# Optimization experiments

Measured on AMD Instinct MI355X. Metric: run time of the kernel, lower is better.

## Reference

```python
import jax, jax.numpy as jnp
import numpy as np

MAX_LENGTH = 128
SOS_TOKEN = 0

V, H, B, S = 16384, 512, 32, 128


def gru_cell(x, h, Wih, Whh, bih, bhh):
    # torch nn.GRU gate layout: [r, z, n]
    gi = x @ Wih.T + bih  # [B, 3H]
    gh = h @ Whh.T + bhh  # [B, 3H]
    ir, iz, inn = jnp.split(gi, 3, axis=-1)
    hr, hz, hn = jnp.split(gh, 3, axis=-1)
    r = jax.nn.sigmoid(ir + hr)
    z = jax.nn.sigmoid(iz + hz)
    n = jnp.tanh(inn + r * hn)
    return (1.0 - z) * n + z * h


def setup_inputs() -> dict:
    key = jax.random.key(0)
    ks = jax.random.split(key, 13)
    w = lambda k, shape: (jax.random.normal(k, shape, dtype=jnp.float32) * 0.1)
    return {
        "input_tensor": jax.random.randint(ks[0], (B, S), 0, V),
        "enc_emb": w(ks[1], (V, H)),
        "enc_Wih": w(ks[2], (3 * H, H)),
        "enc_Whh": w(ks[3], (3 * H, H)),
        "enc_bih": w(ks[4], (3 * H,)),
        "enc_bhh": w(ks[5], (3 * H,)),
        "dec_emb": w(ks[6], (V, H)),
        "dec_Wih": w(ks[7], (3 * H, H)),
        "dec_Whh": w(ks[8], (3 * H, H)),
        "dec_bih": w(ks[9], (3 * H,)),
        "dec_bhh": w(ks[10], (3 * H,)),
        "out_W": w(ks[11], (V, H)),
        "out_b": w(ks[12], (V,)),
    }


def reference(input_tensor, enc_emb, enc_Wih, enc_Whh, enc_bih, enc_bhh,
              dec_emb, dec_Wih, dec_Whh, dec_bih, dec_bhh, out_W, out_b):
    batch = input_tensor.shape[0]

    # ---- encoder: embedding + GRU over source sequence ----
    xs = enc_emb[input_tensor]                 # [B, S, H]
    xs = jnp.swapaxes(xs, 0, 1)                # [S, B, H]

    def enc_step(h, x):
        h = gru_cell(x, h, enc_Wih, enc_Whh, enc_bih, enc_bhh)
        return h, h

    h0 = jnp.zeros((batch, H), dtype=xs.dtype)
    enc_hidden, enc_outputs = jax.lax.scan(enc_step, h0, xs)
    # enc_outputs: [S, B, H] (unused downstream, as in the original)

    # ---- decoder: free-run (target_tensor=None) with argmax feedback ----
    sos = jnp.full((batch,), SOS_TOKEN, dtype=jnp.int32)

    def dec_step(carry, _):
        h, tok = carry
        x = dec_emb[tok]                       # [B, H]
        h = gru_cell(x, h, dec_Wih, dec_Whh, dec_bih, dec_bhh)
        logits = h @ out_W.T + out_b           # [B, V]
        tok = jnp.argmax(logits, axis=-1).astype(jnp.int32)  # topk(1) feedback
        return (h, tok), logits

    (dec_hidden, _), logits = jax.lax.scan(dec_step, (enc_hidden, sos), None,
                                           length=MAX_LENGTH)
    logits = jnp.swapaxes(logits, 0, 1)        # [B, MAX_LENGTH, V]
    log_probs = jax.nn.log_softmax(logits, axis=-1)
    return log_probs, dec_hidden
```

## Files before the change

### kernel.cpp

```cpp
#include <hip/hip_runtime.h>

#define HDIM 512
#define BATCH 32
#define SEQ 128
#define VOCAB 16384
#define NBLK 256
#define NGRU 128
#define NTHR 256
#define SLOTP 32
#define HLDS_W 516

typedef unsigned long long u64;
typedef unsigned int u32;
typedef __attribute__((ext_vector_type(2))) unsigned long long u64x2;

static __device__ __forceinline__ u64 aload64(const u64* p) {
    return __hip_atomic_load(p, __ATOMIC_RELAXED, __HIP_MEMORY_SCOPE_AGENT);
}
static __device__ __forceinline__ void astore64(u64* p, u64 v) {
    __hip_atomic_store(p, v, __ATOMIC_RELAXED, __HIP_MEMORY_SCOPE_AGENT);
}
static __device__ __forceinline__ u32 aload32(const u32* p) {
    return __hip_atomic_load(p, __ATOMIC_RELAXED, __HIP_MEMORY_SCOPE_AGENT);
}
static __device__ __forceinline__ void astore32(u32* p, u32 v) {
    __hip_atomic_store(p, v, __ATOMIC_RELAXED, __HIP_MEMORY_SCOPE_AGENT);
}
static __device__ __forceinline__ void astore32f(float* p, float v) {
    __hip_atomic_store((u32*)p, __float_as_uint(v), __ATOMIC_RELAXED,
                       __HIP_MEMORY_SCOPE_AGENT);
}

static __device__ __forceinline__ float4 ld4(const float* p) {
    return *reinterpret_cast<const float4*>(p);
}
static __device__ __forceinline__ float dot4(float4 a, float4 b) {
    return a.x*b.x + a.y*b.y + a.z*b.z + a.w*b.w;
}
static __device__ __forceinline__ u32 ford(float f) {
    u32 b = __float_as_uint(f);
    return b ^ ((b >> 31) ? 0xFFFFFFFFu : 0x80000000u);
}
static __device__ __forceinline__ u64 shfl_xor_u64(u64 x, int m) {
    int lo = __shfl_xor((int)(u32)x, m);
    int hi = __shfl_xor((int)(u32)(x >> 32), m);
    return ((u64)(u32)hi << 32) | (u32)lo;
}

static __device__ __forceinline__ void pollN(const u32* slots, u32 target,
                                             int tid, int nslots) {
    if (tid < 64) {
        const int per = (nslots + 63) >> 6;
        int it = 0;
        for (;;) {
            bool ok = true;
            for (int k = 0; k < per; ++k) {
                int idx = tid * per + k;
                if (idx < nslots)
                    ok &= (aload32(&slots[idx * SLOTP]) >= target);
            }
            if (__ballot(ok) == ~0ull) break;
            if (it > 64)      __builtin_amdgcn_s_sleep(16);
            else if (it > 8)  __builtin_amdgcn_s_sleep(2);
            ++it;
        }
    }
    __syncthreads();
    asm volatile("" ::: "memory");
}

static __device__ __forceinline__ void poll1(const u32* line, u32 target, int tid) {
    if (tid == 0) {
        int it = 0;
        while (aload32(line) < target) {
            if (it > 64)      __builtin_amdgcn_s_sleep(16);
            else if (it > 8)  __builtin_amdgcn_s_sleep(2);
            ++it;
        }
    }
    __syncthreads();
    asm volatile("" ::: "memory");
}

static __device__ __forceinline__ void stage_wide(float* hlf, const float* hsrc, int tid) {
    #pragma unroll
    for (int g = 0; g < 2; ++g) {
        float4 v[8];
        #pragma unroll
        for (int k = 0; k < 8; ++k) {
            int q = (g * 8 + k) * NTHR + tid;
            asm volatile("global_load_dwordx4 %0, %1, off sc1"
                         : "=v"(v[k]) : "v"(hsrc + q * 4));
        }
        asm volatile("s_waitcnt vmcnt(0)" ::: "memory");
        __builtin_amdgcn_sched_barrier(0);
        #pragma unroll
        for (int k = 0; k < 8; ++k) {
            int q = (g * 8 + k) * NTHR + tid;
            int w = q * 4;
            *reinterpret_cast<float4*>(hlf + (w >> 9) * HLDS_W + (w & 511)) = v[k];
        }
    }
}

static __device__ __forceinline__ void stage_h(float* hlf, const float* hglob, int tid) {
    const u64* src = (const u64*)hglob;
    #pragma unroll
    for (int it = 0; it < 32; ++it) {
        int q = it * 256 + tid;
        int w = q * 2;
        u64 v = aload64(src + q);
        *reinterpret_cast<u64*>(hlf + (w >> 9) * HLDS_W + (w & 511)) = v;
    }
}

static __device__ __forceinline__ void gru_j(
    int j, int tid, const int* toks, const float* hlf, float* hout,
    const float* __restrict__ Wih, const float* __restrict__ Whh,
    const float* __restrict__ bih, const float* __restrict__ bhh,
    const float* __restrict__ emb)
{
    const int lane = tid & 63;
    const int kh   = lane >> 5;
    const int b    = lane & 31;

    const int tok = toks[b];
    const float* xrow = emb + (size_t)tok * HDIM + kh * 256;
    const float* hrow = hlf + b * HLDS_W + kh * 256;
    const float* wir = Wih + (size_t)(0*HDIM + j) * HDIM + kh * 256;
    const float* wiz = Wih + (size_t)(1*HDIM + j) * HDIM + kh * 256;
    const float* win = Wih + (size_t)(2*HDIM + j) * HDIM + kh * 256;
    const float* whr = Whh + (size_t)(0*HDIM + j) * HDIM + kh * 256;
    const float* whz = Whh + (size_t)(1*HDIM + j) * HDIM + kh * 256;
    const float* whn = Whh + (size_t)(2*HDIM + j) * HDIM + kh * 256;

    float pr = 0.f, pz = 0.f, pxn = 0.f, phn = 0.f;
    #pragma unroll 4
    for (int k4 = 0; k4 < 64; ++k4) {
        float4 x4 = ld4(xrow + k4*4);
        float4 h4 = ld4(hrow + k4*4);
        pr  += dot4(x4, ld4(wir + k4*4)) + dot4(h4, ld4(whr + k4*4));
        pz  += dot4(x4, ld4(wiz + k4*4)) + dot4(h4, ld4(whz + k4*4));
        pxn += dot4(x4, ld4(win + k4*4));
        phn += dot4(h4, ld4(whn + k4*4));
    }
    pr  += __shfl_xor(pr, 32);
    pz  += __shfl_xor(pz, 32);
    pxn += __shfl_xor(pxn, 32);
    phn += __shfl_xor(phn, 32);

    if (kh == 0) {
        float r = 1.f / (1.f + expf(-(pr + bih[j]      + bhh[j])));
        float z = 1.f / (1.f + expf(-(pz + bih[HDIM+j] + bhh[HDIM+j])));
        float n = tanhf(pxn + bih[2*HDIM+j] + r * (phn + bhh[2*HDIM+j]));
        float hprev = hlf[b * HLDS_W + j];
        astore32f(hout + b * HDIM + j, (1.f - z) * n + z * hprev);
    }
}

static __device__ __forceinline__ void logits_core(
    int blk, int tid, const float* hlf,
    const float* __restrict__ outW, const float* __restrict__ outb,
    float* __restrict__ out, int t, u64* pk)
{
    const int vloc = tid & 63;
    const int bq   = tid >> 6;
    const int v    = blk * 64 + vloc;
    const float* wrow = outW + (size_t)v * HDIM;

    float acc[4][8];
    #pragma unroll
    for (int q = 0; q < 4; ++q)
        #pragma unroll
        for (int i = 0; i < 8; ++i) acc[q][i] = 0.f;

    #pragma unroll
    for (int q = 0; q < 4; ++q) {
        for (int k4 = 0; k4 < 32; ++k4) {
            float4 w4 = ld4(wrow + q*128 + k4*4);
            #pragma unroll
            for (int i = 0; i < 8; ++i) {
                float4 h4 = ld4(hlf + (bq*8 + i) * HLDS_W + q*128 + k4*4);
                acc[q][i] += dot4(w4, h4);
            }
        }
    }
    const float vbias = outb[v];
    #pragma unroll
    for (int i = 0; i < 8; ++i) {
        const int b = bq*8 + i;
        float s = ((acc[0][i] + acc[1][i]) + acc[2][i]) + acc[3][i] + vbias;
        __builtin_nontemporal_store(s, &out[(size_t)b*(SEQ*VOCAB) + (size_t)t*VOCAB + v]);
        u64 key = ((u64)ford(s) << 32) | (u32)(~(u32)v);
        #pragma unroll
        for (int d = 1; d < 64; d <<= 1) {
            u64 o = shfl_xor_u64(key, d);
            if (o > key) key = o;
        }
        if (vloc == 0) astore64(pk + b * NBLK + blk, key);
    }
}

static __device__ __forceinline__ void argmax_finalize(
    int tid, const u64* pk, u64 (*redk)[8], int* tok_s)
{
    const int fb = tid >> 3, kc = tid & 7;
    const u64* p = pk + fb * NBLK;
    u64 best = aload64(p + kc);
    #pragma unroll 4
    for (int k = 1; k < 32; ++k) {
        u64 x = aload64(p + kc + k * 8);
        if (x > best) best = x;
    }
    redk[fb][kc] = best;
    __syncthreads();
    if (tid < BATCH) {
        u64 bb = redk[tid][0];
        #pragma unroll
        for (int c = 1; c < 8; ++c) { u64 x = redk[tid][c]; if (x > bb) bb = x; }
        tok_s[tid] = (int)(~(u32)bb);
    }
}

static __device__ __forceinline__ void softmax_row(float* p, int tid,
                                                   float* redm, float* reds) {
    float4 vals[16];
    float m = -3.4e38f;
    #pragma unroll
    for (int i = 0; i < 16; ++i) {
        vals[i] = ld4(p + (i * 256 + tid) * 4);
        m = fmaxf(m, fmaxf(fmaxf(vals[i].x, vals[i].y), fmaxf(vals[i].z, vals[i].w)));
    }
    #pragma unroll
    for (int d = 1; d < 64; d <<= 1) m = fmaxf(m, __shfl_xor(m, d));
    if ((tid & 63) == 0) redm[tid >> 6] = m;
    __syncthreads();
    m = fmaxf(fmaxf(redm[0], redm[1]), fmaxf(redm[2], redm[3]));
    float s = 0.f;
    #pragma unroll
    for (int i = 0; i < 16; ++i) {
        s += expf(vals[i].x - m) + expf(vals[i].y - m)
           + expf(vals[i].z - m) + expf(vals[i].w - m);
    }
    #pragma unroll
    for (int d = 1; d < 64; d <<= 1) s += __shfl_xor(s, d);
    if ((tid & 63) == 0) reds[tid >> 6] = s;
    __syncthreads();
    s = reds[0] + reds[1] + reds[2] + reds[3];
    const float lg = m + logf(s);
    #pragma unroll
    for (int i = 0; i < 16; ++i) {
        float4 r;
        r.x = vals[i].x - lg; r.y = vals[i].y - lg;
        r.z = vals[i].z - lg; r.w = vals[i].w - lg;
        *reinterpret_cast<float4*>(p + (i * 256 + tid) * 4) = r;
    }
    __syncthreads();
}

__global__ __launch_bounds__(NTHR, 1) void seq2seq_main(
    const int* __restrict__ input,
    const float* __restrict__ enc_emb, const float* __restrict__ enc_Wih,
    const float* __restrict__ enc_Whh, const float* __restrict__ enc_bih,
    const float* __restrict__ enc_bhh,
    const float* __restrict__ dec_emb, const float* __restrict__ dec_Wih,
    const float* __restrict__ dec_Whh, const float* __restrict__ dec_bih,
    const float* __restrict__ dec_bhh,
    const float* __restrict__ out_W, const float* __restrict__ out_b,
    float* __restrict__ out, float* hglob, u64* pk,
    u32* hslot, u32* pkslot, u32* go_h, u32* go_pk, u64* tokline)
{
    __shared__ __align__(16) float hl[BATCH][HLDS_W];
    __shared__ int tok_s[BATCH];

    const int tid = threadIdx.x;
    const int blk = blockIdx.x;
    float* hlf = &hl[0][0];

    for (int i = tid; i < BATCH * HLDS_W; i += NTHR) hlf[i] = 0.f;
    __syncthreads();

    const int w = tid >> 6;

    if (blk < NGRU) {
        for (int t = 0; t < SEQ; ++t) {
            float* hgo = hglob + ((t + 1) & 1) * (BATCH * HDIM);
            if (tid < BATCH) tok_s[tid] = input[tid * SEQ + t];
            __syncthreads();
            gru_j(blk * 4 + w, tid, tok_s, hlf, hgo,
                  enc_Wih, enc_Whh, enc_bih, enc_bhh, enc_emb);
            __syncthreads();
            if (tid == 0) astore32(&hslot[blk * SLOTP], (u32)(t + 1));
            poll1(go_h, (u32)(t + 1), tid);
            stage_wide(hlf, hgo, tid);
            __syncthreads();
        }
    } else if (blk == 255) {
        for (int t = 0; t < SEQ; ++t) {
            pollN(hslot, (u32)(t + 1), tid, NGRU);
            if (tid == 0) astore32(go_h, (u32)(t + 1));
        }
    }

    for (int t = 0; t < SEQ; ++t) {
        float* hgo = hglob + ((t + 1) & 1) * (BATCH * HDIM);

        if (blk < NGRU) {
            if (t == 0) {
                if (tid < BATCH) tok_s[tid] = 0;
                __syncthreads();
            } else {
                if (blk < BATCH) {
                    poll1(go_pk, (u32)t, tid);
                    if (tid < 64) {
                        const u64* prow = pk + (size_t)blk * NBLK + tid * 4;
                        u64x2 a, b2;
                        asm volatile("global_load_dwordx4 %0, %1, off sc1"
                                     : "=v"(a) : "v"(prow));
                        asm volatile("global_load_dwordx4 %0, %1, off sc1"
                                     : "=v"(b2) : "v"(prow + 2));
                        asm volatile("s_waitcnt vmcnt(0)" ::: "memory");
                        u64 best = a.x;
                        if (a.y  > best) best = a.y;
                        if (b2.x > best) best = b2.x;
                        if (b2.y > best) best = b2.y;
                        #pragma unroll
                        for (int d = 1; d < 64; d <<= 1) {
                            u64 o = shfl_xor_u64(best, d);
                            if (o > best) best = o;
                        }
                        if (tid == 0)
                            astore64(&tokline[blk * 16],
                                     ((u64)(u32)t << 32) | (u32)(~(u32)best));
                    }
                }
                if (tid < 64) {
                    u64 tv = 0; int it = 0;
                    for (;;) {
                        bool ok = true;
                        if (tid < 32) {
                            tv = aload64(&tokline[tid * 16]);
                            ok = ((u32)(tv >> 32) >= (u32)t);
                        }
                        if (__ballot(ok) == ~0ull) break;
                        if (it > 64)      __builtin_amdgcn_s_sleep(16);
                        else if (it > 8)  __builtin_amdgcn_s_sleep(2);
                        ++it;
                    }
                    if (tid < 32) tok_s[tid] = (int)(u32)tv;
                }
                __syncthreads();
            }
            gru_j(blk * 4 + w, tid, tok_s, hlf, hgo,
                  dec_Wih, dec_Whh, dec_bih, dec_bhh, dec_emb);
            __syncthreads();
            if (tid == 0) astore32(&hslot[blk * SLOTP], (u32)(SEQ + t + 1));
        }

        if (blk == 255) {
            pollN(hslot, (u32)(SEQ + t + 1), tid, NGRU);
            if (tid == 0) astore32(go_h, (u32)(SEQ + t + 1));
        } else {
            poll1(go_h, (u32)(SEQ + t + 1), tid);
        }
        stage_wide(hlf, hgo, tid);
        __syncthreads();
        logits_core(blk, tid, hlf, out_W, out_b, out, t, pk);
        __syncthreads();
        if (tid == 0) astore32(&pkslot[blk * SLOTP], (u32)(t + 1));
        if (blk == 254) {
            pollN(pkslot, (u32)(t + 1), tid, NBLK);
            if (tid == 0) astore32(go_pk, (u32)(t + 1));
        }
    }

    if (blk < 16) {
        const int idx = blk * 1024 + tid * 4;
        const int b = idx >> 9, j = idx & 511;
        *reinterpret_cast<float4*>(out + (size_t)BATCH * SEQ * VOCAB + idx) =
            *reinterpret_cast<const float4*>(&hl[b][j]);
    }
}

__global__ __launch_bounds__(256) void init_kernel(float* __restrict__ h0,
                                                   u32* __restrict__ hslot,
                                                   u32* __restrict__ pkslot,
                                                   u32* __restrict__ extra) {
    int i = blockIdx.x * 256 + threadIdx.x;
    if (i < BATCH * HDIM) h0[i] = 0.f;
    if (i < NGRU * SLOTP) hslot[i] = 0;
    if (i < NBLK * SLOTP) pkslot[i] = 0;
    if (i < 1088) extra[i] = 0;
}

__global__ __launch_bounds__(256) void gru_step_fb(
    const float* __restrict__ h_in, float* __restrict__ h_out,
    const float* __restrict__ Wih, const float* __restrict__ Whh,
    const float* __restrict__ bih, const float* __restrict__ bhh,
    const float* __restrict__ emb,
    const int* __restrict__ enc_tokens, int t, const u64* __restrict__ pk)
{
    __shared__ __align__(16) float hlt[BATCH][HLDS_W];
    __shared__ int tok_s[BATCH];
    __shared__ u64 redk[BATCH][8];
    const int tid = threadIdx.x;

    if (enc_tokens != nullptr) {
        if (tid < BATCH) tok_s[tid] = enc_tokens[tid * SEQ + t];
    } else if (t == 0) {
        if (tid < BATCH) tok_s[tid] = 0;
    } else {
        argmax_finalize(tid, pk, redk, tok_s);
    }
    stage_h(&hlt[0][0], h_in, tid);
    __syncthreads();
    gru_j(blockIdx.x * 4 + (tid >> 6), tid, tok_s, &hlt[0][0], h_out,
          Wih, Whh, bih, bhh, emb);
}

__global__ __launch_bounds__(256) void logits_fb(
    const float* __restrict__ h, const float* __restrict__ outW,
    const float* __restrict__ outb, float* __restrict__ out,
    int t, u64* __restrict__ pk)
{
    __shared__ __align__(16) float hlt[BATCH][HLDS_W];
    const int tid = threadIdx.x;
    stage_h(&hlt[0][0], h, tid);
    __syncthreads();
    logits_core(blockIdx.x, tid, &hlt[0][0], outW, outb, out, t, pk);
}

__global__ __launch_bounds__(256) void copy_fb(const float* __restrict__ src,
                                               float* __restrict__ dst, int n) {
    int i = blockIdx.x * 256 + threadIdx.x;
    if (i < n) dst[i] = src[i];
}

__global__ __launch_bounds__(256) void softmax_kernel(float* __restrict__ out) {
    __shared__ float redm[4];
    __shared__ float reds[4];
    softmax_row(out + (size_t)blockIdx.x * VOCAB, threadIdx.x, redm, reds);
}

extern "C" void kernel_launch(void* const* d_in, const int* in_sizes, int n_in,
                              void* d_out, int out_size, void* d_ws, size_t ws_size,
                              hipStream_t stream) {
    const int*   input    = (const int*)  d_in[0];
    const float* enc_emb  = (const float*)d_in[1];
    const float* enc_Wih  = (const float*)d_in[2];
    const float* enc_Whh  = (const float*)d_in[3];
    const float* enc_bih  = (const float*)d_in[4];
    const float* enc_bhh  = (const float*)d_in[5];
    const float* dec_emb  = (const float*)d_in[6];
    const float* dec_Wih  = (const float*)d_in[7];
    const float* dec_Whh  = (const float*)d_in[8];
    const float* dec_bih  = (const float*)d_in[9];
    const float* dec_bhh  = (const float*)d_in[10];
    const float* out_W    = (const float*)d_in[11];
    const float* out_b    = (const float*)d_in[12];

    float* out = (float*)d_out;
    char*  ws  = (char*)d_ws;

    float* hglob   = (float*)ws;
    u64*   pk      = (u64*)(ws + 131072);
    u32*   hslot   = (u32*)(ws + 196608);
    u32*   pkslot  = (u32*)(ws + 212992);
    u32*   extra   = (u32*)(ws + 245760);
    u32*   go_h    = extra;
    u32*   go_pk   = extra + SLOTP;
    u64*   tokline = (u64*)(extra + 2 * SLOTP);

    init_kernel<<<dim3(64), dim3(256), 0, stream>>>(hglob, hslot, pkslot, extra);

    void* args[] = {
        (void*)&input, (void*)&enc_emb, (void*)&enc_Wih, (void*)&enc_Whh,
        (void*)&enc_bih, (void*)&enc_bhh,
        (void*)&dec_emb, (void*)&dec_Wih, (void*)&dec_Whh, (void*)&dec_bih,
        (void*)&dec_bhh, (void*)&out_W, (void*)&out_b,
        (void*)&out, (void*)&hglob, (void*)&pk,
        (void*)&hslot, (void*)&pkslot, (void*)&go_h, (void*)&go_pk, (void*)&tokline
    };
    hipError_t rc = hipLaunchCooperativeKernel((void*)seq2seq_main,
                                               dim3(NBLK), dim3(NTHR),
                                               args, 0, stream);
    if (rc != hipSuccess) {
        float* hb[2] = { hglob, hglob + BATCH * HDIM };
        for (int t = 0; t < SEQ; ++t) {
            gru_step_fb<<<dim3(128), dim3(256), 0, stream>>>(
                hb[t & 1], hb[(t + 1) & 1],
                enc_Wih, enc_Whh, enc_bih, enc_bhh, enc_emb, input, t, nullptr);
        }
        for (int t = 0; t < SEQ; ++t) {
            gru_step_fb<<<dim3(128), dim3(256), 0, stream>>>(
                hb[t & 1], hb[(t + 1) & 1],
                dec_Wih, dec_Whh, dec_bih, dec_bhh, dec_emb, nullptr, t, pk);
            logits_fb<<<dim3(NBLK), dim3(256), 0, stream>>>(
                hb[(t + 1) & 1], out_W, out_b, out, t, pk);
        }
        copy_fb<<<dim3((BATCH * HDIM + 255) / 256), dim3(256), 0, stream>>>(
            hglob, out + (size_t)BATCH * SEQ * VOCAB, BATCH * HDIM);
    }

    softmax_kernel<<<dim3(BATCH * SEQ), dim3(256), 0, stream>>>(out);
}
```

Before: 10.17 ms.

## Replace aggregator-block barriers with epoch-tagged argmax keys and direct slot polling

Removes the dedicated aggregator blocks that gathered per-block completion flags and republished a single go flag. GRU blocks now poll all hidden-state slots directly. The partial-argmax keys carry the timestep in their high bits, so the batch-finalizer blocks spin on the key data itself instead of waiting on a separate pkslot/go_pk barrier. The aim is to cut one relay hop of latency from each of the 256 sequential steps. The cost is more polling traffic from many blocks and fewer bits for the float ordering key (32 bits shifted into a 46-bit window, with 14 bits for the index), which still preserves ordering.

```diff
diff --git a/kernel.cpp b/kernel.cpp
--- a/kernel.cpp
+++ b/kernel.cpp
@@ -45,6 +45,10 @@
     int lo = __shfl_xor((int)(u32)x, m);
     int hi = __shfl_xor((int)(u32)(x >> 32), m);
     return ((u64)(u32)hi << 32) | (u32)lo;
+}
+
+static __device__ __forceinline__ u64 mkkey(int t, float s, int v) {
+    return ((u64)(u32)(t + 1) << 46) | ((u64)ford(s) << 14) | (u32)(16383 - v);
 }
 
 static __device__ __forceinline__ void pollN(const u32* slots, u32 target,
@@ -69,19 +73,6 @@
     asm volatile("" ::: "memory");
 }
 
-static __device__ __forceinline__ void poll1(const u32* line, u32 target, int tid) {
-    if (tid == 0) {
-        int it = 0;
-        while (aload32(line) < target) {
-            if (it > 64)      __builtin_amdgcn_s_sleep(16);
-            else if (it > 8)  __builtin_amdgcn_s_sleep(2);
-            ++it;
-        }
-    }
-    __syncthreads();
-    asm volatile("" ::: "memory");
-}
-
 static __device__ __forceinline__ void stage_wide(float* hlf, const float* hsrc, int tid) {
     #pragma unroll
     for (int g = 0; g < 2; ++g) {
@@ -191,7 +182,7 @@
         const int b = bq*8 + i;
         float s = ((acc[0][i] + acc[1][i]) + acc[2][i]) + acc[3][i] + vbias;
         __builtin_nontemporal_store(s, &out[(size_t)b*(SEQ*VOCAB) + (size_t)t*VOCAB + v]);
-        u64 key = ((u64)ford(s) << 32) | (u32)(~(u32)v);
+        u64 key = mkkey(t, s, v);
         #pragma unroll
         for (int d = 1; d < 64; d <<= 1) {
             u64 o = shfl_xor_u64(key, d);
@@ -218,7 +209,7 @@
         u64 bb = redk[tid][0];
         #pragma unroll
         for (int c = 1; c < 8; ++c) { u64 x = redk[tid][c]; if (x > bb) bb = x; }
-        tok_s[tid] = (int)(~(u32)bb);
+        tok_s[tid] = 16383 - (int)(bb & 0x3FFF);
     }
 }
 
@@ -268,7 +259,7 @@
     const float* __restrict__ dec_bhh,
     const float* __restrict__ out_W, const float* __restrict__ out_b,
     float* __restrict__ out, float* hglob, u64* pk,
-    u32* hslot, u32* pkslot, u32* go_h, u32* go_pk, u64* tokline)
+    u32* hslot, u64* tokline)
 {
     __shared__ __align__(16) float hl[BATCH][HLDS_W];
     __shared__ int tok_s[BATCH];
@@ -291,14 +282,9 @@
                   enc_Wih, enc_Whh, enc_bih, enc_bhh, enc_emb);
             __syncthreads();
             if (tid == 0) astore32(&hslot[blk * SLOTP], (u32)(t + 1));
-            poll1(go_h, (u32)(t + 1), tid);
+            pollN(hslot, (u32)(t + 1), tid, NGRU);
             stage_wide(hlf, hgo, tid);
             __syncthreads();
-        }
-    } else if (blk == 255) {
-        for (int t = 0; t < SEQ; ++t) {
-            pollN(hslot, (u32)(t + 1), tid, NGRU);
-            if (tid == 0) astore32(go_h, (u32)(t + 1));
         }
     }
 
@@ -311,15 +297,26 @@
                 __syncthreads();
             } else {
                 if (blk < BATCH) {
-                    poll1(go_pk, (u32)t, tid);
                     if (tid < 64) {
                         const u64* prow = pk + (size_t)blk * NBLK + tid * 4;
                         u64x2 a, b2;
-                        asm volatile("global_load_dwordx4 %0, %1, off sc1"
-                                     : "=v"(a) : "v"(prow));
-                        asm volatile("global_load_dwordx4 %0, %1, off sc1"
-                                     : "=v"(b2) : "v"(prow + 2));
-                        asm volatile("s_waitcnt vmcnt(0)" ::: "memory");
+                        const u32 ep = (u32)t;
+                        int it = 0;
+                        for (;;) {
+                            asm volatile("global_load_dwordx4 %0, %1, off sc1"
+                                         : "=v"(a) : "v"(prow));
+                            asm volatile("global_load_dwordx4 %0, %1, off sc1"
+                                         : "=v"(b2) : "v"(prow + 2));
+                            asm volatile("s_waitcnt vmcnt(0)" ::: "memory");
+                            bool ok = ((u32)(a.x  >> 46) == ep) &&
+                                      ((u32)(a.y  >> 46) == ep) &&
+                                      ((u32)(b2.x >> 46) == ep) &&
+                                      ((u32)(b2.y >> 46) == ep);
+                            if (__ballot(ok) == ~0ull) break;
+                            if (it > 64)      __builtin_amdgcn_s_sleep(16);
+                            else if (it > 8)  __builtin_amdgcn_s_sleep(2);
+                            ++it;
+                        }
                         u64 best = a.x;
                         if (a.y  > best) best = a.y;
                         if (b2.x > best) best = b2.x;
@@ -331,7 +328,8 @@
                         }
                         if (tid == 0)
                             astore64(&tokline[blk * 16],
-                                     ((u64)(u32)t << 32) | (u32)(~(u32)best));
+                                     ((u64)(u32)t << 32) |
+                                     (u32)(16383 - (u32)(best & 0x3FFF)));
                     }
                 }
                 if (tid < 64) {
@@ -357,21 +355,10 @@
             if (tid == 0) astore32(&hslot[blk * SLOTP], (u32)(SEQ + t + 1));
         }
 
-        if (blk == 255) {
-            pollN(hslot, (u32)(SEQ + t + 1), tid, NGRU);
-            if (tid == 0) astore32(go_h, (u32)(SEQ + t + 1));
-        } else {
-            poll1(go_h, (u32)(SEQ + t + 1), tid);
-        }
+        pollN(hslot, (u32)(SEQ + t + 1), tid, NGRU);
         stage_wide(hlf, hgo, tid);
         __syncthreads();
         logits_core(blk, tid, hlf, out_W, out_b, out, t, pk);
-        __syncthreads();
-        if (tid == 0) astore32(&pkslot[blk * SLOTP], (u32)(t + 1));
-        if (blk == 254) {
-            pollN(pkslot, (u32)(t + 1), tid, NBLK);
-            if (tid == 0) astore32(go_pk, (u32)(t + 1));
-        }
     }
 
     if (blk < 16) {
@@ -384,13 +371,13 @@
 
 __global__ __launch_bounds__(256) void init_kernel(float* __restrict__ h0,
                                                    u32* __restrict__ hslot,
-                                                   u32* __restrict__ pkslot,
-                                                   u32* __restrict__ extra) {
+                                                   u32* __restrict__ pk32,
+                                                   u32* __restrict__ tokl32) {
     int i = blockIdx.x * 256 + threadIdx.x;
     if (i < BATCH * HDIM) h0[i] = 0.f;
     if (i < NGRU * SLOTP) hslot[i] = 0;
-    if (i < NBLK * SLOTP) pkslot[i] = 0;
-    if (i < 1088) extra[i] = 0;
+    if (i < 16384) pk32[i] = 0;
+    if (i < 1024) tokl32[i] = 0;
 }
 
 __global__ __launch_bounds__(256) void gru_step_fb(
@@ -465,13 +452,10 @@
     float* hglob   = (float*)ws;
     u64*   pk      = (u64*)(ws + 131072);
     u32*   hslot   = (u32*)(ws + 196608);
-    u32*   pkslot  = (u32*)(ws + 212992);
-    u32*   extra   = (u32*)(ws + 245760);
-    u32*   go_h    = extra;
-    u32*   go_pk   = extra + SLOTP;
-    u64*   tokline = (u64*)(extra + 2 * SLOTP);
-
-    init_kernel<<<dim3(64), dim3(256), 0, stream>>>(hglob, hslot, pkslot, extra);
+    u64*   tokline = (u64*)(ws + 212992);
+
+    init_kernel<<<dim3(64), dim3(256), 0, stream>>>(hglob, hslot,
+                                                    (u32*)pk, (u32*)tokline);
 
     void* args[] = {
         (void*)&input, (void*)&enc_emb, (void*)&enc_Wih, (void*)&enc_Whh,
@@ -479,7 +463,7 @@
         (void*)&dec_emb, (void*)&dec_Wih, (void*)&dec_Whh, (void*)&dec_bih,
         (void*)&dec_bhh, (void*)&out_W, (void*)&out_b,
         (void*)&out, (void*)&hglob, (void*)&pk,
-        (void*)&hslot, (void*)&pkslot, (void*)&go_h, (void*)&go_pk, (void*)&tokline
+        (void*)&hslot, (void*)&tokline
     };
     hipError_t rc = hipLaunchCooperativeKernel((void*)seq2seq_main,
                                                dim3(NBLK), dim3(NTHR),
```

After: 9.313 ms, median of 2. 8.4% less time.
